# Kernel tuning notes

Measured on AMD Instinct MI355X. Metric: run time of the kernel, lower is better.

The kernel has to match this reference:

```python
import jax, jax.numpy as jnp
import numpy as np

DIM = 1024
NUM_HEADS = 16
HEAD_DIM = 64
SCALE = 1.0 / np.sqrt(float(HEAD_DIM))


def setup_inputs() -> dict:
    key = jax.random.key(0)
    ks = jax.random.split(key, 11)
    B, S, D = 2, 4096, DIM
    glorot = lambda k, shape: jax.random.uniform(
        k, shape, jnp.float32,
        -jnp.sqrt(6.0 / (shape[0] + shape[1])), jnp.sqrt(6.0 / (shape[0] + shape[1])))
    return {
        "x": jax.random.normal(ks[0], (B, S, D), jnp.float32),
        "Wq": glorot(ks[1], (D, NUM_HEADS * HEAD_DIM)),
        "bq": jnp.zeros((NUM_HEADS * HEAD_DIM,), jnp.float32),
        "Wk": glorot(ks[2], (D, NUM_HEADS * HEAD_DIM)),
        "bk": jnp.zeros((NUM_HEADS * HEAD_DIM,), jnp.float32),
        "Wv": glorot(ks[3], (D, NUM_HEADS * HEAD_DIM)),
        "bv": jnp.zeros((NUM_HEADS * HEAD_DIM,), jnp.float32),
        "Wqt": glorot(ks[4], (D, D)),
        "bqt": jnp.zeros((D,), jnp.float32),
        "Wo": glorot(ks[5], (D, D)),
        "bo": jnp.zeros((D,), jnp.float32),
        "num_anchor_tokens": 512,
    }


def _split_heads(t):
    # [B, T, H*Dh] -> [B, H, T, Dh]
    B, T, _ = t.shape
    return t.reshape(B, T, NUM_HEADS, HEAD_DIM).transpose(0, 2, 1, 3)


def reference(x, Wq, bq, Wk, bk, Wv, bv, Wqt, bqt, Wo, bo, num_anchor_tokens):
    B, S, D = x.shape
    A = num_anchor_tokens  # static Python int
    anchors = x[:, :A, :]            # [B, A, D]
    queries = x[:, A:, :]            # [B, S-A, D]

    anchor_q = _split_heads(anchors @ Wq + bq)   # [B, H, A, Dh]
    anchor_k = _split_heads(anchors @ Wk + bk)   # [B, H, A, Dh]
    anchor_v = _split_heads(anchors @ Wv + bv)   # [B, H, A, Dh]
    query_q = _split_heads(queries @ Wqt + bqt)  # [B, H, S-A, Dh]

    combined_q = jnp.concatenate([anchor_q, query_q], axis=2)  # [B, H, S, Dh]
    scores = jnp.einsum("bhsd,bhad->bhsa", combined_q, anchor_k) * SCALE
    attn = jax.nn.softmax(scores, axis=-1)        # [B, H, S, A]
    out = jnp.einsum("bhsa,bhad->bhsd", attn, anchor_v)  # [B, H, S, Dh]
    out = out.transpose(0, 2, 1, 3).reshape(B, S, D)
    return out @ Wo + bo
```

## Files before the change

### kernel.cpp

```cpp
#include <hip/hip_runtime.h>
#include <hip/hip_bf16.h>
#include <math.h>
#include <stdint.h>

typedef _Float16 f16;
typedef _Float16 f16x8 __attribute__((ext_vector_type(8)));
typedef _Float16 f16x4 __attribute__((ext_vector_type(4)));
typedef _Float16 f16x2 __attribute__((ext_vector_type(2)));
typedef float f32x4 __attribute__((ext_vector_type(4)));

#define DIM   1024
#define NH    16
#define HD    64
#define BB    2
#define SS    4096
#define AA    512
#define SCALE 0.125f
#define EXP_C1 0.18033688011112043f
#define EXP_C2 (-2.8853900817779268f)

#define GLOAD_LDS16(g, l)                                                                   \
  __builtin_amdgcn_global_load_lds((const __attribute__((address_space(1))) uint32_t*)(g),  \
                                   (__attribute__((address_space(3))) uint32_t*)(l), 16, 0, 0)

static const size_t OFF_XH  = 0;
static const size_t OFF_WT  = 8388608;
static const size_t OFF_QC  = OFF_WT + 5u*1048576u;
static const size_t OFF_KB  = OFF_QC + 8388608u;
static const size_t OFF_VT  = OFF_KB + 1048576u;
static const size_t OFF_AO  = OFF_VT + 1048576u;

__global__ __launch_bounds__(256) void cast_x_kernel(const float* __restrict__ x,
                                                     f16* __restrict__ xh) {
    size_t i = ((size_t)blockIdx.x * 256 + threadIdx.x) * 4;
    float4 v = *reinterpret_cast<const float4*>(x + i);
    f16x4 o;
    o[0] = (f16)v.x; o[1] = (f16)v.y; o[2] = (f16)v.z; o[3] = (f16)v.w;
    *reinterpret_cast<f16x4*>(xh + i) = o;
}

__global__ __launch_bounds__(256) void wcast_kernel(const float* W0, const float* W1,
                                                    const float* W2, const float* W3,
                                                    const float* W4,
                                                    f16* T0, f16* T1, f16* T2, f16* T3, f16* T4) {
    __shared__ float tile[32][33];
    const float* W; f16* T;
    switch (blockIdx.z) {
        case 0: W = W0; T = T0; break;
        case 1: W = W1; T = T1; break;
        case 2: W = W2; T = T2; break;
        case 3: W = W3; T = T3; break;
        default: W = W4; T = T4; break;
    }
    int tx = threadIdx.x, ty = threadIdx.y;
    int gx = blockIdx.x * 32, gy = blockIdx.y * 32;
#pragma unroll
    for (int i = 0; i < 32; i += 8)
        tile[ty + i][tx] = W[(size_t)(gy + ty + i) * DIM + gx + tx];
    __syncthreads();
#pragma unroll
    for (int i = 0; i < 32; i += 8)
        T[(size_t)(gx + ty + i) * DIM + gy + tx] = (f16)tile[tx][ty + i];
}

#define G_STAGE(buf, k0)                                               \
    {                                                                  \
        GLOAD_LDS16(Ap + (k0), &As[buf][wid << 9]);                    \
        GLOAD_LDS16(Ap + (k0) + (size_t)64 * DIM,                      \
                    &As[buf][(wid << 9) + 2048]);                      \
        GLOAD_LDS16(Bp + (k0), &Bs[buf][wid << 9]);                    \
        GLOAD_LDS16(Bp + (k0) + (size_t)64 * DIM,                      \
                    &Bs[buf][(wid << 9) + 2048]);                      \
    }

#define G_KLOOP                                                                                   \
    G_STAGE(0, 0);                                                                                \
    __syncthreads();                                                                              \
    int cur = 0;                                                                                  \
    for (int k0 = 0; k0 < DIM; k0 += 32) {                                                        \
        if (k0 + 32 < DIM) G_STAGE(cur ^ 1, k0 + 32);                                             \
        f16x8 af[4], bf[4];                                                                       \
        _Pragma("unroll")                                                                         \
        for (int m = 0; m < 4; m++) {                                                             \
            const int r = wr + m * 16 + lr;                                                       \
            af[m] = *reinterpret_cast<const f16x8*>(&As[cur][r * 32 + ((lg ^ ((r >> 1) & 3)) << 3)]); \
        }                                                                                         \
        _Pragma("unroll")                                                                         \
        for (int n = 0; n < 4; n++) {                                                             \
            const int r = wc + n * 16 + lr;                                                       \
            bf[n] = *reinterpret_cast<const f16x8*>(&Bs[cur][r * 32 + ((lg ^ ((r >> 1) & 3)) << 3)]); \
        }                                                                                         \
        _Pragma("unroll")                                                                         \
        for (int m = 0; m < 4; m++)                                                               \
            _Pragma("unroll")                                                                     \
            for (int n = 0; n < 4; n++)                                                           \
                acc[m][n] = __builtin_amdgcn_mfma_f32_16x16x32_f16(af[m], bf[n], acc[m][n], 0, 0, 0); \
        __syncthreads();                                                                          \
        cur ^= 1;                                                                                 \
    }

__global__ __launch_bounds__(256) void proj_kernel(const f16* __restrict__ xh,
                                                   const f16* __restrict__ wtq,
                                                   const f16* __restrict__ wtqt,
                                                   const f16* __restrict__ wtk,
                                                   const f16* __restrict__ wtv,
                                                   const float* __restrict__ bq,
                                                   const float* __restrict__ bqt,
                                                   const float* __restrict__ bk,
                                                   const float* __restrict__ bv,
                                                   f16* __restrict__ qc,
                                                   f16* __restrict__ kbuf,
                                                   f16* __restrict__ vtb) {
    __shared__ __align__(16) f16 As[2][4096];
    __shared__ __align__(16) f16 Bs[2][4096];

    const int t    = threadIdx.x;
    const int wid  = t >> 6;
    const int lane = t & 63;
    const int lr   = lane & 15;
    const int lg   = lane >> 4;
    const int x    = blockIdx.x, bc = blockIdx.y;

    int b, srow0, mode, sdim;
    const f16* Bt; const float* bias; f16* outp;
    if (x < 64) {
        b = x >> 5; srow0 = (x & 31) * 128;
        if (srow0 < 512) { Bt = wtq; bias = bq; } else { Bt = wtqt; bias = bqt; }
        mode = 0; sdim = SS; outp = qc;
    } else if (x < 72) {
        int y = x - 64; b = y >> 2; srow0 = (y & 3) * 128;
        Bt = wtk; bias = bk; mode = 0; sdim = AA; outp = kbuf;
    } else {
        int y = x - 72; b = y >> 2; srow0 = (y & 3) * 128;
        Bt = wtv; bias = bv; mode = 1; sdim = AA; outp = vtb;
    }

    const int srow = (wid << 4) + (lane >> 2);
    const int sch  = ((lane & 3) ^ ((lane >> 3) & 3)) << 3;
    const f16* Ap = xh + ((size_t)b * SS + srow0 + srow) * DIM + sch;
    const f16* Bp = Bt + ((size_t)(bc * 128 + srow)) * DIM + sch;

    const int wr = (wid >> 1) * 64;
    const int wc = (wid & 1) * 64;

    f32x4 acc[4][4] = {};
    G_KLOOP

#pragma unroll
    for (int m = 0; m < 4; m++) {
        const int row_local = wr + m * 16 + lg * 4;
#pragma unroll
        for (int n = 0; n < 4; n++) {
            const int c  = bc * 128 + wc + n * 16 + lr;
            const float bvv = bias[c];
            const int h = c >> 6, d = c & 63;
#pragma unroll
            for (int q = 0; q < 4; q++) {
                const int s_g = srow0 + row_local + q;
                const float val = acc[m][n][q] + bvv;
                if (mode == 0)
                    outp[(((size_t)(b * NH + h)) * sdim + s_g) * HD + d] = (f16)val;
                else
                    outp[(((size_t)(b * NH + h)) * HD + d) * AA + s_g] = (f16)val;
            }
        }
    }
}

__global__ __launch_bounds__(256) void final_gemm(const f16* __restrict__ ao,
                                                  const f16* __restrict__ wto,
                                                  const float* __restrict__ bo,
                                                  float* __restrict__ out) {
    __shared__ __align__(16) f16 As[2][4096];
    __shared__ __align__(16) f16 Bs[2][4096];

    const int t    = threadIdx.x;
    const int wid  = t >> 6;
    const int lane = t & 63;
    const int lr   = lane & 15;
    const int lg   = lane >> 4;
    const int br   = blockIdx.x, bc = blockIdx.y;

    const int b     = br >> 5;
    const int srow0 = (br & 31) * 128;

    const int srow = (wid << 4) + (lane >> 2);
    const int sch  = ((lane & 3) ^ ((lane >> 3) & 3)) << 3;
    const f16* Ap = ao + ((size_t)b * SS + srow0 + srow) * DIM + sch;
    const f16* Bp = wto + ((size_t)(bc * 128 + srow)) * DIM + sch;

    const int wr = (wid >> 1) * 64;
    const int wc = (wid & 1) * 64;

    f32x4 acc[4][4] = {};
    G_KLOOP

#pragma unroll
    for (int m = 0; m < 4; m++) {
        const int row_local = wr + m * 16 + lg * 4;
#pragma unroll
        for (int n = 0; n < 4; n++) {
            const int c  = bc * 128 + wc + n * 16 + lr;
            const float bvv = bo[c];
#pragma unroll
            for (int q = 0; q < 4; q++)
                out[((size_t)b * SS + srow0 + row_local + q) * DIM + c] = acc[m][n][q] + bvv;
        }
    }
}

__global__ __launch_bounds__(256) void attn_kernel(const f16* __restrict__ qc,
                                                   const f16* __restrict__ kb,
                                                   const f16* __restrict__ vt,
                                                   f16* __restrict__ ao) {
    __shared__ __align__(16) f16 Ks[2][64 * 64];
    __shared__ __align__(16) f16 Vs[2][64 * 64];
    __shared__ __align__(16) f16 Ps[4][16][64];

    const int t    = threadIdx.x;
    const int wid  = t >> 6;
    const int lane = t & 63;
    const int lr   = lane & 15;
    const int lg   = lane >> 4;
    const int qt   = blockIdx.x;
    const int h    = blockIdx.y;
    const int b    = blockIdx.z;
    const size_t bh = (size_t)b * NH + h;

    const int qrow = qt * 64 + wid * 16 + lr;
    const f16* qp = qc + (bh * SS + qrow) * HD + lg * 8;
    const f16x8 qa0 = *reinterpret_cast<const f16x8*>(qp);
    const f16x8 qa1 = *reinterpret_cast<const f16x8*>(qp + 32);

    const int sr_k = wid * 16 + (lane >> 3);
    const f16* kg = kb + bh * (size_t)AA * HD;
    const f16* vg = vt + bh * (size_t)HD * AA;

    f32x4 acc[4] = {};
    float rsum[4] = {0.f, 0.f, 0.f, 0.f};

#define ATTN_STAGE(buf, a0)                                                          \
    {                                                                                \
        _Pragma("unroll")                                                            \
        for (int i = 0; i < 2; i++) {                                                \
            const int r  = sr_k + i * 8;                                             \
            const int ck = (((lane & 7) ^ (r & 7)) << 3);                            \
            GLOAD_LDS16(kg + (size_t)((a0) + r) * HD + ck,                           \
                        &Ks[buf][(wid * 16 + i * 8) * 64]);                          \
            GLOAD_LDS16(vg + (size_t)r * AA + (a0) + ck,                             \
                        &Vs[buf][(wid * 16 + i * 8) * 64]);                          \
        }                                                                            \
    }

    ATTN_STAGE(0, 0);
    asm volatile("s_waitcnt vmcnt(0)");
    __syncthreads();

    int cur = 0;
    for (int at = 0; at < AA / 64; ++at) {
        if (at < AA / 64 - 1) ATTN_STAGE(cur ^ 1, (at + 1) * 64);

        f32x4 s[4];
#pragma unroll
        for (int n = 0; n < 4; n++) {
            const int r = n * 16 + lr;
            const int x = r & 7;
            f16x8 kf0 = *reinterpret_cast<const f16x8*>(&Ks[cur][r * 64 + ((lg ^ x) << 3)]);
            f16x8 kf1 = *reinterpret_cast<const f16x8*>(&Ks[cur][r * 64 + (((lg + 4) ^ x) << 3)]);
            f32x4 z = {};
            z = __builtin_amdgcn_mfma_f32_16x16x32_f16(qa0, kf0, z, 0, 0, 0);
            z = __builtin_amdgcn_mfma_f32_16x16x32_f16(qa1, kf1, z, 0, 0, 0);
            s[n] = z;
        }

#pragma unroll
        for (int n = 0; n < 4; n++) {
#pragma unroll
            for (int q = 0; q < 4; q++) {
                const float p = exp2f(fmaf(s[n][q], EXP_C1, EXP_C2));
                rsum[q] += p;
                const int row = lg * 4 + q;
                Ps[wid][row][(((2 * n + (lr >> 3)) ^ (row & 7)) << 3) + (lr & 7)] = (f16)p;
            }
        }
        const f16x8 pa0 = *reinterpret_cast<const f16x8*>(&Ps[wid][lr][(lg ^ (lr & 7)) << 3]);
        const f16x8 pa1 = *reinterpret_cast<const f16x8*>(&Ps[wid][lr][((lg + 4) ^ (lr & 7)) << 3]);

#pragma unroll
        for (int n = 0; n < 4; n++) {
            const int d = n * 16 + lr;
            const int x = d & 7;
            f16x8 vf0 = *reinterpret_cast<const f16x8*>(&Vs[cur][d * 64 + ((lg ^ x) << 3)]);
            f16x8 vf1 = *reinterpret_cast<const f16x8*>(&Vs[cur][d * 64 + (((lg + 4) ^ x) << 3)]);
            acc[n] = __builtin_amdgcn_mfma_f32_16x16x32_f16(pa0, vf0, acc[n], 0, 0, 0);
            acc[n] = __builtin_amdgcn_mfma_f32_16x16x32_f16(pa1, vf1, acc[n], 0, 0, 0);
        }

        asm volatile("s_waitcnt vmcnt(0)");
        __syncthreads();
        cur ^= 1;
    }

#pragma unroll
    for (int off = 1; off < 16; off <<= 1) {
#pragma unroll
        for (int q = 0; q < 4; q++) rsum[q] += __shfl_xor(rsum[q], off);
    }
#pragma unroll
    for (int q = 0; q < 4; q++) {
        const float inv = 1.0f / rsum[q];
        const int row = qt * 64 + wid * 16 + lg * 4 + q;
#pragma unroll
        for (int n = 0; n < 4; n++) {
            ao[((size_t)b * SS + row) * DIM + h * HD + n * 16 + lr] = (f16)(acc[n][q] * inv);
        }
    }
}

extern "C" void kernel_launch(void* const* d_in, const int* in_sizes, int n_in,
                              void* d_out, int out_size, void* d_ws, size_t ws_size,
                              hipStream_t stream) {
    const float* x   = (const float*)d_in[0];
    const float* Wq  = (const float*)d_in[1];
    const float* bq  = (const float*)d_in[2];
    const float* Wk  = (const float*)d_in[3];
    const float* bk  = (const float*)d_in[4];
    const float* Wv  = (const float*)d_in[5];
    const float* bv  = (const float*)d_in[6];
    const float* Wqt = (const float*)d_in[7];
    const float* bqt = (const float*)d_in[8];
    const float* Wo  = (const float*)d_in[9];
    const float* bo  = (const float*)d_in[10];

    f16* ws   = (f16*)d_ws;
    f16* xh   = ws + OFF_XH;
    f16* wtq  = ws + OFF_WT;
    f16* wtk  = wtq + 1048576u;
    f16* wtv  = wtk + 1048576u;
    f16* wtqt = wtv + 1048576u;
    f16* wto  = wtqt + 1048576u;
    f16* qc   = ws + OFF_QC;
    f16* kbuf = ws + OFF_KB;
    f16* vtb  = ws + OFF_VT;
    f16* ao   = ws + OFF_AO;

    cast_x_kernel<<<8192, 256, 0, stream>>>(x, xh);
    wcast_kernel<<<dim3(32, 32, 5), dim3(32, 8), 0, stream>>>(Wq, Wk, Wv, Wqt, Wo,
                                                              wtq, wtk, wtv, wtqt, wto);

    proj_kernel<<<dim3(80, 8), 256, 0, stream>>>(xh, wtq, wtqt, wtk, wtv,
                                                 bq, bqt, bk, bv, qc, kbuf, vtb);

    attn_kernel<<<dim3(64, NH, BB), 256, 0, stream>>>(qc, kbuf, vtb, ao);

    final_gemm<<<dim3(64, 8), 256, 0, stream>>>(ao, wto, bo, (float*)d_out);
}
```

Measured before the change: 122.4 us.

## Merge cast kernels, deepen final GEMM K-tile to 64, skip last attn sync

Folds the x cast and the weight transpose-cast into one launch that dispatches on block index, removing one kernel launch. The final output GEMM now stages 64-wide K tiles with an 8-chunk XOR swizzle, doing two MFMA sub-steps per barrier and halving the number of k-loop iterations and syncs. The cost is doubled LDS use, which may lower occupancy. The attention loop also skips the wait and barrier on its last iteration.

Result: faster. 118.2 us (-3.4%).

```diff
diff --git a/kernel.cpp b/kernel.cpp
--- a/kernel.cpp
+++ b/kernel.cpp
@@ -6,7 +6,6 @@
 typedef _Float16 f16;
 typedef _Float16 f16x8 __attribute__((ext_vector_type(8)));
 typedef _Float16 f16x4 __attribute__((ext_vector_type(4)));
-typedef _Float16 f16x2 __attribute__((ext_vector_type(2)));
 typedef float f32x4 __attribute__((ext_vector_type(4)));
 
 #define DIM   1024
@@ -30,30 +29,35 @@
 static const size_t OFF_VT  = OFF_KB + 1048576u;
 static const size_t OFF_AO  = OFF_VT + 1048576u;
 
-__global__ __launch_bounds__(256) void cast_x_kernel(const float* __restrict__ x,
-                                                     f16* __restrict__ xh) {
-    size_t i = ((size_t)blockIdx.x * 256 + threadIdx.x) * 4;
-    float4 v = *reinterpret_cast<const float4*>(x + i);
-    f16x4 o;
-    o[0] = (f16)v.x; o[1] = (f16)v.y; o[2] = (f16)v.z; o[3] = (f16)v.w;
-    *reinterpret_cast<f16x4*>(xh + i) = o;
-}
-
-__global__ __launch_bounds__(256) void wcast_kernel(const float* W0, const float* W1,
-                                                    const float* W2, const float* W3,
-                                                    const float* W4,
-                                                    f16* T0, f16* T1, f16* T2, f16* T3, f16* T4) {
+__global__ __launch_bounds__(256) void prep_kernel(const float* __restrict__ x,
+                                                   f16* __restrict__ xh,
+                                                   const float* W0, const float* W1,
+                                                   const float* W2, const float* W3,
+                                                   const float* W4,
+                                                   f16* T0, f16* T1, f16* T2, f16* T3, f16* T4) {
     __shared__ float tile[32][33];
+    const int bid = blockIdx.x;
+    const int t   = threadIdx.x;
+    if (bid < 8192) {
+        size_t i = ((size_t)bid * 256 + t) * 4;
+        float4 v = *reinterpret_cast<const float4*>(x + i);
+        f16x4 o;
+        o[0] = (f16)v.x; o[1] = (f16)v.y; o[2] = (f16)v.z; o[3] = (f16)v.w;
+        *reinterpret_cast<f16x4*>(xh + i) = o;
+        return;
+    }
+    const int bid2 = bid - 8192;
     const float* W; f16* T;
-    switch (blockIdx.z) {
+    switch (bid2 >> 10) {
         case 0: W = W0; T = T0; break;
         case 1: W = W1; T = T1; break;
         case 2: W = W2; T = T2; break;
         case 3: W = W3; T = T3; break;
         default: W = W4; T = T4; break;
     }
-    int tx = threadIdx.x, ty = threadIdx.y;
-    int gx = blockIdx.x * 32, gy = blockIdx.y * 32;
+    const int rem = bid2 & 1023;
+    const int gx = (rem & 31) << 5, gy = (rem >> 5) << 5;
+    const int tx = t & 31, ty = t >> 5;
 #pragma unroll
     for (int i = 0; i < 32; i += 8)
         tile[ty + i][tx] = W[(size_t)(gy + ty + i) * DIM + gx + tx];
@@ -167,12 +171,23 @@
     }
 }
 
+#define G_STAGE64(buf, k0)                                                     \
+    {                                                                          \
+        _Pragma("unroll")                                                      \
+        for (int i = 0; i < 4; i++) {                                          \
+            GLOAD_LDS16(Ap + (k0) + (size_t)(i * 32) * DIM,                    \
+                        &As[buf][i * 2048 + (wid << 9)]);                      \
+            GLOAD_LDS16(Bp + (k0) + (size_t)(i * 32) * DIM,                    \
+                        &Bs[buf][i * 2048 + (wid << 9)]);                      \
+        }                                                                      \
+    }
+
 __global__ __launch_bounds__(256) void final_gemm(const f16* __restrict__ ao,
                                                   const f16* __restrict__ wto,
                                                   const float* __restrict__ bo,
                                                   float* __restrict__ out) {
-    __shared__ __align__(16) f16 As[2][4096];
-    __shared__ __align__(16) f16 Bs[2][4096];
+    __shared__ __align__(16) f16 As[2][8192];
+    __shared__ __align__(16) f16 Bs[2][8192];
 
     const int t    = threadIdx.x;
     const int wid  = t >> 6;
@@ -184,8 +199,8 @@
     const int b     = br >> 5;
     const int srow0 = (br & 31) * 128;
 
-    const int srow = (wid << 4) + (lane >> 2);
-    const int sch  = ((lane & 3) ^ ((lane >> 3) & 3)) << 3;
+    const int srow = (wid << 3) + (lane >> 3);
+    const int sch  = ((lane & 7) ^ (lane >> 3)) << 3;
     const f16* Ap = ao + ((size_t)b * SS + srow0 + srow) * DIM + sch;
     const f16* Bp = wto + ((size_t)(bc * 128 + srow)) * DIM + sch;
 
@@ -193,7 +208,36 @@
     const int wc = (wid & 1) * 64;
 
     f32x4 acc[4][4] = {};
-    G_KLOOP
+
+    G_STAGE64(0, 0);
+    __syncthreads();
+    int cur = 0;
+    for (int k0 = 0; k0 < DIM; k0 += 64) {
+        if (k0 + 64 < DIM) G_STAGE64(cur ^ 1, k0 + 64);
+#pragma unroll
+        for (int ks = 0; ks < 2; ks++) {
+            f16x8 af[4], bf[4];
+#pragma unroll
+            for (int m = 0; m < 4; m++) {
+                const int r = wr + m * 16 + lr;
+                af[m] = *reinterpret_cast<const f16x8*>(
+                    &As[cur][r * 64 + ((((ks << 2) + lg) ^ (lr & 7)) << 3)]);
+            }
+#pragma unroll
+            for (int n = 0; n < 4; n++) {
+                const int r = wc + n * 16 + lr;
+                bf[n] = *reinterpret_cast<const f16x8*>(
+                    &Bs[cur][r * 64 + ((((ks << 2) + lg) ^ (lr & 7)) << 3)]);
+            }
+#pragma unroll
+            for (int m = 0; m < 4; m++)
+#pragma unroll
+                for (int n = 0; n < 4; n++)
+                    acc[m][n] = __builtin_amdgcn_mfma_f32_16x16x32_f16(af[m], bf[n], acc[m][n], 0, 0, 0);
+        }
+        __syncthreads();
+        cur ^= 1;
+    }
 
 #pragma unroll
     for (int m = 0; m < 4; m++) {
@@ -296,8 +340,10 @@
             acc[n] = __builtin_amdgcn_mfma_f32_16x16x32_f16(pa1, vf1, acc[n], 0, 0, 0);
         }
 
-        asm volatile("s_waitcnt vmcnt(0)");
-        __syncthreads();
+        if (at < AA / 64 - 1) {
+            asm volatile("s_waitcnt vmcnt(0)");
+            __syncthreads();
+        }
         cur ^= 1;
     }
 
@@ -344,9 +390,8 @@
     f16* vtb  = ws + OFF_VT;
     f16* ao   = ws + OFF_AO;
 
-    cast_x_kernel<<<8192, 256, 0, stream>>>(x, xh);
-    wcast_kernel<<<dim3(32, 32, 5), dim3(32, 8), 0, stream>>>(Wq, Wk, Wv, Wqt, Wo,
-                                                              wtq, wtk, wtv, wtqt, wto);
+    prep_kernel<<<8192 + 5120, 256, 0, stream>>>(x, xh, Wq, Wk, Wv, Wqt, Wo,
+                                                 wtq, wtk, wtv, wtqt, wto);
 
     proj_kernel<<<dim3(80, 8), 256, 0, stream>>>(xh, wtq, wtqt, wtk, wtv,
                                                  bq, bqt, bk, bv, qc, kbuf, vtb);
```
